# Performance work log

Hardware: AMD Instinct MI355X
Metric: run time of the kernel (lower is better)

The kernel has to match this reference:

```python
import jax, jax.numpy as jnp
import numpy as np

H = 1024        # hidden_size
E = 8           # num_experts
K = 2           # experts_per_token
I = 1024        # intermediate_size (mlp1 outputs 2*I, interleaved gate/linear)
N = 4096        # n_tokens
ALPHA = 1.702
LIMIT = 7.0
EPS = 1e-5


def setup_inputs() -> dict:
    key = jax.random.key(0)
    ks = jax.random.split(key, 5)
    x = jax.random.normal(ks[0], (N, H), jnp.float32)
    norm_scale = jnp.ones((H,), jnp.float32)
    gate_w = jax.random.normal(ks[1], (H, E), jnp.float32) * 0.02
    gate_b = jnp.zeros((E,), jnp.float32)
    mlp1_w = jax.random.normal(ks[2], (E, 2 * I, H), jnp.float32) * 0.02
    mlp1_b = jnp.zeros((E, 2 * I), jnp.float32)
    mlp2_w = jax.random.normal(ks[3], (E, H, I), jnp.float32) * 0.02
    mlp2_b = jnp.zeros((E, H), jnp.float32)
    return {"x": x, "norm_scale": norm_scale, "gate_w": gate_w, "gate_b": gate_b,
            "mlp1_w": mlp1_w, "mlp1_b": mlp1_b, "mlp2_w": mlp2_w, "mlp2_b": mlp2_b}


def _swiglu(h):
    # even indices = gate, odd indices = linear (interleaved)
    x_g = jnp.minimum(h[..., ::2], LIMIT)           # clip gate above only
    x_l = jnp.clip(h[..., 1::2], -LIMIT, LIMIT)     # clip linear both sides
    return x_g * jax.nn.sigmoid(ALPHA * x_g) * (x_l + 1.0)


def reference(x, norm_scale, gate_w, gate_b, mlp1_w, mlp1_b, mlp2_w, mlp2_b):
    # RMSNorm (fp32)
    t = x * jax.lax.rsqrt(jnp.mean(x * x, axis=-1, keepdims=True) + EPS) * norm_scale
    # Router: top-k gating with softmax over selected logits
    g = t @ gate_w + gate_b                          # [N, E]
    logits, idx = jax.lax.top_k(g, K)                # [N, K]
    w = jax.nn.softmax(logits, axis=-1)              # [N, K]
    n = x.shape[0]
    # Scatter routing weights into dense combine matrix [N, E]
    # (top_k indices are unique per row, so .set is exact)
    combine = jnp.zeros((n, E), x.dtype).at[jnp.arange(n)[:, None], idx].set(w)
    # Per-expert SwiGLU MLP over all tokens, weighted combine + residual.
    # Loop over the small fixed expert count (E=8); avoids materializing the
    # huge [N, K, 2I, H] gathered-weight tensor from the original gather path.
    out = x
    for e in range(E):
        h1 = _swiglu(t @ mlp1_w[e].T + mlp1_b[e])    # [N, I]
        h2 = h1 @ mlp2_w[e].T + mlp2_b[e]            # [N, H]
        out = out + combine[:, e:e + 1] * h2
    return out
```

## Files before the change

kernel.cpp:

```cpp
#include <hip/hip_runtime.h>
#include <hip/hip_bf16.h>
#include <stdint.h>

#define HDIM 1024
#define NEXP 8
#define TOPK 2
#define IDIM 1024
#define TWO_I 2048
#define ALPHA 1.702f
#define LIMIT 7.0f
#define EPS 1e-5f

#define BM 128
#define BN 128
#define BK 64

typedef __attribute__((ext_vector_type(8))) short bf16x8;
typedef __attribute__((ext_vector_type(4))) float f32x4;

typedef __attribute__((address_space(1))) const uint32_t g_u32;
typedef __attribute__((address_space(3))) uint32_t l_u32;

__device__ __forceinline__ void load_lds16(const void* g, void* l) {
    __builtin_amdgcn_global_load_lds((g_u32*)g, (l_u32*)l, 16, 0, 0);
}

__device__ __forceinline__ ushort f2bf(float f) {
    union { float f; uint32_t u; } v{f};
    uint32_t u = v.u;
    return (ushort)((u + 0x7fffu + ((u >> 16) & 1u)) >> 16);
}

__global__ __launch_bounds__(256) void k_f32_to_bf16(const float* __restrict__ src,
                                                     ushort* __restrict__ dst, int n4) {
    int i = blockIdx.x * blockDim.x + threadIdx.x;
    int stride = gridDim.x * blockDim.x;
    for (; i < n4; i += stride) {
        float4 v = reinterpret_cast<const float4*>(src)[i];
        ushort4 o;
        o.x = f2bf(v.x); o.y = f2bf(v.y); o.z = f2bf(v.z); o.w = f2bf(v.w);
        reinterpret_cast<ushort4*>(dst)[i] = o;
    }
}

__global__ __launch_bounds__(256) void k_conv_w1(const float* __restrict__ src,
                                                 ushort* __restrict__ dst) {
    const int b = blockIdx.x;
    const int e = b >> 11;
    const int j = b & 2047;
    const int dj = ((j & 1) << 10) | (j >> 1);
    const float4* s = reinterpret_cast<const float4*>(src + (size_t)b * HDIM);
    ushort4* d = reinterpret_cast<ushort4*>(dst + ((size_t)e * TWO_I + dj) * HDIM);
    float4 v = s[threadIdx.x];
    ushort4 o;
    o.x = f2bf(v.x); o.y = f2bf(v.y); o.z = f2bf(v.z); o.w = f2bf(v.w);
    d[threadIdx.x] = o;
}

__global__ __launch_bounds__(256) void k_norm_router(
    const float* __restrict__ x, const float* __restrict__ scale,
    const float* __restrict__ gw, const float* __restrict__ gb,
    ushort* __restrict__ t_bf, float* __restrict__ route_w,
    int* __restrict__ counts, int* __restrict__ bucket, int n_tok)
{
    const int n = blockIdx.x;
    const int tid = threadIdx.x;
    const int lane = tid & 63, wid = tid >> 6;

    __shared__ float red[4];
    __shared__ float gred[4][NEXP];

    const float4 xv = reinterpret_cast<const float4*>(x + (size_t)n * HDIM)[tid];
    float ss = xv.x * xv.x + xv.y * xv.y + xv.z * xv.z + xv.w * xv.w;
    #pragma unroll
    for (int off = 32; off; off >>= 1) ss += __shfl_down(ss, off, 64);
    if (lane == 0) red[wid] = ss;
    __syncthreads();
    const float tot = red[0] + red[1] + red[2] + red[3];
    const float rms = rsqrtf(tot / (float)HDIM + EPS);

    const float4 sv = reinterpret_cast<const float4*>(scale)[tid];
    float t0 = xv.x * rms * sv.x;
    float t1 = xv.y * rms * sv.y;
    float t2 = xv.z * rms * sv.z;
    float t3 = xv.w * rms * sv.w;

    ushort4 tb;
    tb.x = f2bf(t0); tb.y = f2bf(t1); tb.z = f2bf(t2); tb.w = f2bf(t3);
    reinterpret_cast<ushort4*>(t_bf + (size_t)n * HDIM)[tid] = tb;

    float g[NEXP];
    #pragma unroll
    for (int e = 0; e < NEXP; ++e) g[e] = 0.f;
    const float tv[4] = {t0, t1, t2, t3};
    const float4* gwv = reinterpret_cast<const float4*>(gw);
    #pragma unroll
    for (int j = 0; j < 4; ++j) {
        const int h = tid * 4 + j;
        const float4 a = gwv[h * 2 + 0];
        const float4 b = gwv[h * 2 + 1];
        g[0] += tv[j] * a.x; g[1] += tv[j] * a.y; g[2] += tv[j] * a.z; g[3] += tv[j] * a.w;
        g[4] += tv[j] * b.x; g[5] += tv[j] * b.y; g[6] += tv[j] * b.z; g[7] += tv[j] * b.w;
    }
    #pragma unroll
    for (int e = 0; e < NEXP; ++e) {
        #pragma unroll
        for (int off = 32; off; off >>= 1) g[e] += __shfl_down(g[e], off, 64);
    }
    if (lane == 0) {
        #pragma unroll
        for (int e = 0; e < NEXP; ++e) gred[wid][e] = g[e];
    }
    __syncthreads();

    if (tid == 0) {
        float gg[NEXP];
        #pragma unroll
        for (int e = 0; e < NEXP; ++e)
            gg[e] = gred[0][e] + gred[1][e] + gred[2][e] + gred[3][e] + gb[e];
        int i0 = 0; float l0 = gg[0];
        #pragma unroll
        for (int e = 1; e < NEXP; ++e) if (gg[e] > l0) { l0 = gg[e]; i0 = e; }
        int i1 = -1; float l1 = -3.4e38f;
        #pragma unroll
        for (int e = 0; e < NEXP; ++e) if (e != i0 && gg[e] > l1) { l1 = gg[e]; i1 = e; }
        const float w0 = 1.f / (1.f + __expf(l1 - l0));
        const float w1 = 1.f - w0;
        route_w[n * 2 + 0] = w0;
        route_w[n * 2 + 1] = w1;
        int p0 = atomicAdd(&counts[i0], 1);
        bucket[i0 * n_tok + p0] = n * 2 + 0;
        int p1 = atomicAdd(&counts[i1], 1);
        bucket[i1 * n_tok + p1] = n * 2 + 1;
    }
}

__global__ __launch_bounds__(256) void k_gemm1(
    const ushort* __restrict__ tA, const ushort* __restrict__ w1bf,
    const float* __restrict__ b1,
    const int* __restrict__ counts, const int* __restrict__ bucket,
    ushort* __restrict__ h1, int n_tok, int rt_max)
{
    const int bx = blockIdx.x;
    const int rt = bx >> 7;
    const int e  = (bx >> 4) & 7;
    const int jt = bx & 15;
    const int cnt = counts[e];
    if (rt * BM >= cnt) return;

    __shared__ __align__(16) ushort As[2][BM * BK];
    __shared__ __align__(16) ushort Bs[2][BN * BK];

    const int tid = threadIdx.x;
    const int lane = tid & 63, wid = tid >> 6;
    const int wm = wid >> 1, wn = wid & 1;

    int tokrow[4];
    #pragma unroll
    for (int it = 0; it < 4; ++it) {
        int pos = rt * BM + it * 32 + (tid >> 3);
        tokrow[it] = bucket[e * n_tok + min(pos, cnt - 1)] >> 1;
    }
    const ushort* wbase = w1bf + (size_t)e * TWO_I * HDIM;
    const ushort* bsrc[4];
    #pragma unroll
    for (int it = 0; it < 4; ++it) {
        int br = it * 32 + (tid >> 3);
        int G = br >> 4, r16 = br & 15;
        int half = (G >> 1) & 1;
        int sub = ((G >> 2) << 1) | (G & 1);
        int srcrow = half * IDIM + jt * 64 + sub * 16 + r16;
        bsrc[it] = wbase + (size_t)srcrow * HDIM;
    }
    const int swz = (((tid & 7) ^ ((tid >> 3) & 7)) * 8);

    f32x4 acc[4][4];
    #pragma unroll
    for (int mi = 0; mi < 4; ++mi)
        #pragma unroll
        for (int ni = 0; ni < 4; ++ni) acc[mi][ni] = (f32x4)0.f;

    auto stage = [&](int buf, int kt) {
        const int k0 = kt * BK + swz;
        #pragma unroll
        for (int it = 0; it < 4; ++it)
            load_lds16(tA + (size_t)tokrow[it] * HDIM + k0, &As[buf][(it * 32 + wid * 8) * BK]);
        #pragma unroll
        for (int it = 0; it < 4; ++it)
            load_lds16(bsrc[it] + k0, &Bs[buf][(it * 32 + wid * 8) * BK]);
    };
    auto compute = [&](int buf) {
        #pragma unroll
        for (int kk = 0; kk < 2; ++kk) {
            bf16x8 a[4], b[4];
            #pragma unroll
            for (int mi = 0; mi < 4; ++mi) {
                int r = wm * 64 + mi * 16 + (lane & 15);
                int off = r * BK + (((kk * 4 + (lane >> 4)) ^ (lane & 7)) * 8);
                a[mi] = *reinterpret_cast<const bf16x8*>(&As[buf][off]);
            }
            #pragma unroll
            for (int ni = 0; ni < 4; ++ni) {
                int r = wn * 64 + ni * 16 + (lane & 15);
                int off = r * BK + (((kk * 4 + (lane >> 4)) ^ (lane & 7)) * 8);
                b[ni] = *reinterpret_cast<const bf16x8*>(&Bs[buf][off]);
            }
            #pragma unroll
            for (int mi = 0; mi < 4; ++mi)
                #pragma unroll
                for (int ni = 0; ni < 4; ++ni)
                    acc[mi][ni] = __builtin_amdgcn_mfma_f32_16x16x32_bf16(a[mi], b[ni], acc[mi][ni], 0, 0, 0);
        }
    };

    stage(0, 0);
    __syncthreads();
    int cur = 0;
    for (int kt = 0; kt < HDIM / BK; ++kt) {
        if (kt + 1 < HDIM / BK) stage(cur ^ 1, kt + 1);
        compute(cur);
        __syncthreads();
        cur ^= 1;
    }

    int ent[4][4];
    #pragma unroll
    for (int mi = 0; mi < 4; ++mi)
        #pragma unroll
        for (int r = 0; r < 4; ++r) {
            int pos = rt * BM + wm * 64 + mi * 16 + (lane >> 4) * 4 + r;
            ent[mi][r] = (pos < cnt) ? bucket[e * n_tok + pos] : -1;
        }
    #pragma unroll
    for (int ni = 0; ni < 2; ++ni) {
        const int col = jt * 64 + (wn * 2 + ni) * 16 + (lane & 15);
        const float bg = b1[e * TWO_I + 2 * col];
        const float bl = b1[e * TWO_I + 2 * col + 1];
        #pragma unroll
        for (int mi = 0; mi < 4; ++mi) {
            const f32x4 vg = acc[mi][ni];
            const f32x4 vl = acc[mi][ni + 2];
            #pragma unroll
            for (int r = 0; r < 4; ++r) {
                if (ent[mi][r] >= 0) {
                    const float xg = fminf(vg[r] + bg, LIMIT);
                    const float xl = fminf(fmaxf(vl[r] + bl, -LIMIT), LIMIT);
                    const float s = 1.f / (1.f + __expf(-ALPHA * xg));
                    h1[(size_t)ent[mi][r] * IDIM + col] = f2bf(xg * s * (xl + 1.f));
                }
            }
        }
    }
}

__global__ __launch_bounds__(256) void k_gemm2(
    const ushort* __restrict__ h1, const ushort* __restrict__ w2bf,
    const float* __restrict__ b2, const float* __restrict__ route_w,
    const int* __restrict__ counts, const int* __restrict__ bucket,
    float* __restrict__ contrib, int n_tok, int rt_max)
{
    const int bx = blockIdx.x;
    const int rt = bx >> 6;
    const int e  = (bx >> 3) & 7;
    const int ct = bx & 7;
    const int cnt = counts[e];
    if (rt * BM >= cnt) return;
    const int c0 = ct * BN;

    __shared__ __align__(16) ushort As[2][BM * BK];
    __shared__ __align__(16) ushort Bs[2][BN * BK];

    const int tid = threadIdx.x;
    const int lane = tid & 63, wid = tid >> 6;
    const int wm = wid >> 1, wn = wid & 1;

    int rowent[4];
    #pragma unroll
    for (int it = 0; it < 4; ++it) {
        int pos = rt * BM + it * 32 + (tid >> 3);
        rowent[it] = bucket[e * n_tok + min(pos, cnt - 1)];
    }
    const ushort* wB = w2bf + (size_t)e * HDIM * IDIM;
    const int swz = (((tid & 7) ^ ((tid >> 3) & 7)) * 8);

    f32x4 acc[4][4];
    #pragma unroll
    for (int mi = 0; mi < 4; ++mi)
        #pragma unroll
        for (int ni = 0; ni < 4; ++ni) acc[mi][ni] = (f32x4)0.f;

    auto stage = [&](int buf, int kt) {
        const int k0 = kt * BK + swz;
        #pragma unroll
        for (int it = 0; it < 4; ++it)
            load_lds16(h1 + (size_t)rowent[it] * IDIM + k0, &As[buf][(it * 32 + wid * 8) * BK]);
        #pragma unroll
        for (int it = 0; it < 4; ++it)
            load_lds16(wB + (size_t)(c0 + it * 32 + (tid >> 3)) * IDIM + k0, &Bs[buf][(it * 32 + wid * 8) * BK]);
    };
    auto compute = [&](int buf) {
        #pragma unroll
        for (int kk = 0; kk < 2; ++kk) {
            bf16x8 a[4], b[4];
            #pragma unroll
            for (int mi = 0; mi < 4; ++mi) {
                int r = wm * 64 + mi * 16 + (lane & 15);
                int off = r * BK + (((kk * 4 + (lane >> 4)) ^ (lane & 7)) * 8);
                a[mi] = *reinterpret_cast<const bf16x8*>(&As[buf][off]);
            }
            #pragma unroll
            for (int ni = 0; ni < 4; ++ni) {
                int r = wn * 64 + ni * 16 + (lane & 15);
                int off = r * BK + (((kk * 4 + (lane >> 4)) ^ (lane & 7)) * 8);
                b[ni] = *reinterpret_cast<const bf16x8*>(&Bs[buf][off]);
            }
            #pragma unroll
            for (int mi = 0; mi < 4; ++mi)
                #pragma unroll
                for (int ni = 0; ni < 4; ++ni)
                    acc[mi][ni] = __builtin_amdgcn_mfma_f32_16x16x32_bf16(a[mi], b[ni], acc[mi][ni], 0, 0, 0);
        }
    };

    stage(0, 0);
    __syncthreads();
    int cur = 0;
    for (int kt = 0; kt < IDIM / BK; ++kt) {
        if (kt + 1 < IDIM / BK) stage(cur ^ 1, kt + 1);
        compute(cur);
        __syncthreads();
        cur ^= 1;
    }

    int ent[4][4];
    float wgt[4][4];
    #pragma unroll
    for (int mi = 0; mi < 4; ++mi)
        #pragma unroll
        for (int r = 0; r < 4; ++r) {
            int pos = rt * BM + wm * 64 + mi * 16 + (lane >> 4) * 4 + r;
            if (pos < cnt) {
                ent[mi][r] = bucket[e * n_tok + pos];
                wgt[mi][r] = route_w[ent[mi][r]];
            } else ent[mi][r] = -1;
        }
    #pragma unroll
    for (int ni = 0; ni < 4; ++ni) {
        const int c = c0 + wn * 64 + ni * 16 + (lane & 15);
        const float bc = b2[e * HDIM + c];
        #pragma unroll
        for (int mi = 0; mi < 4; ++mi) {
            const f32x4 v = acc[mi][ni];
            #pragma unroll
            for (int r = 0; r < 4; ++r) {
                if (ent[mi][r] >= 0) {
                    const int tok = ent[mi][r] >> 1, slot = ent[mi][r] & 1;
                    contrib[((size_t)slot * n_tok + tok) * HDIM + c] = wgt[mi][r] * (v[r] + bc);
                }
            }
        }
    }
}

__global__ __launch_bounds__(256) void k_combine(
    const float* __restrict__ x, const float* __restrict__ contrib,
    float* __restrict__ out, int n4, int slot_stride4)
{
    int i = blockIdx.x * blockDim.x + threadIdx.x;
    if (i >= n4) return;
    float4 xv = reinterpret_cast<const float4*>(x)[i];
    float4 c0 = reinterpret_cast<const float4*>(contrib)[i];
    float4 c1 = reinterpret_cast<const float4*>(contrib)[i + slot_stride4];
    float4 o;
    o.x = xv.x + c0.x + c1.x;
    o.y = xv.y + c0.y + c1.y;
    o.z = xv.z + c0.z + c1.z;
    o.w = xv.w + c0.w + c1.w;
    reinterpret_cast<float4*>(out)[i] = o;
}

extern "C" void kernel_launch(void* const* d_in, const int* in_sizes, int n_in,
                              void* d_out, int out_size, void* d_ws, size_t ws_size,
                              hipStream_t stream) {
    const float* x    = (const float*)d_in[0];
    const float* nsc  = (const float*)d_in[1];
    const float* gw   = (const float*)d_in[2];
    const float* gb   = (const float*)d_in[3];
    const float* w1   = (const float*)d_in[4];
    const float* b1   = (const float*)d_in[5];
    const float* w2   = (const float*)d_in[6];
    const float* b2   = (const float*)d_in[7];
    float* out = (float*)d_out;

    const int N = in_sizes[0] / HDIM;
    const int rt_max = (N + BM - 1) / BM;

    uintptr_t p = (uintptr_t)d_ws;
    auto carve = [&p](size_t bytes) { uintptr_t q = p; p += (bytes + 255) & ~(size_t)255; return q; };
    ushort* t_bf    = (ushort*)carve((size_t)N * HDIM * 2);
    ushort* w1bf    = (ushort*)carve((size_t)NEXP * TWO_I * HDIM * 2);
    ushort* w2bf    = (ushort*)carve((size_t)NEXP * HDIM * IDIM * 2);
    ushort* h1      = (ushort*)carve((size_t)N * TOPK * IDIM * 2);
    float*  contrib = (float*)carve((size_t)TOPK * N * HDIM * 4);
    float*  route_w = (float*)carve((size_t)N * TOPK * 4);
    int*    bucket  = (int*)carve((size_t)NEXP * N * 4);
    int*    counts  = (int*)carve(256);

    hipMemsetAsync(counts, 0, NEXP * sizeof(int), stream);

    k_conv_w1<<<NEXP * TWO_I, 256, 0, stream>>>(w1, w1bf);
    const int n4w2 = NEXP * HDIM * IDIM / 4;
    k_f32_to_bf16<<<2048, 256, 0, stream>>>(w2, w2bf, n4w2);

    k_norm_router<<<N, 256, 0, stream>>>(x, nsc, gw, gb, t_bf, route_w, counts, bucket, N);

    k_gemm1<<<rt_max * NEXP * (TWO_I / BN), 256, 0, stream>>>(t_bf, w1bf, b1, counts, bucket, h1, N, rt_max);
    k_gemm2<<<rt_max * NEXP * (HDIM / BN), 256, 0, stream>>>(h1, w2bf, b2, route_w, counts, bucket, contrib, N, rt_max);

    const int n4 = N * HDIM / 4;
    k_combine<<<(n4 + 255) / 256, 256, 0, stream>>>(x, contrib, out, n4, n4);
}
```

Measured before the change: 407.7 us.

## Split norm/router into wave-per-token gating and ballot-based bucketing kernel

The fused norm+router kernel, which used one 256-thread block per token and two global atomics per token, is replaced by two kernels. The first processes one token per wave, uses xor-shuffle reductions with no shared memory or block syncs, and writes expert indices to a new buffer. The second builds the per-expert buckets with wave ballots, a prefix scan in shared memory, and one atomic per expert per block. This removes heavy global atomic contention on eight counters and the per-token block syncs, at the cost of an extra kernel launch and a small intermediate buffer. The bucket order is now deterministic per block.

Measured after the change: 337.7 us. 1.21x faster.

```diff
diff --git a/kernel.cpp b/kernel.cpp
--- a/kernel.cpp
+++ b/kernel.cpp
@@ -57,81 +57,138 @@
     d[threadIdx.x] = o;
 }
 
-__global__ __launch_bounds__(256) void k_norm_router(
+__global__ __launch_bounds__(256) void k_norm_gate(
     const float* __restrict__ x, const float* __restrict__ scale,
     const float* __restrict__ gw, const float* __restrict__ gb,
     ushort* __restrict__ t_bf, float* __restrict__ route_w,
-    int* __restrict__ counts, int* __restrict__ bucket, int n_tok)
+    int* __restrict__ eidx, int n_tok)
 {
-    const int n = blockIdx.x;
+    const int tok = blockIdx.x * 4 + (threadIdx.x >> 6);
+    if (tok >= n_tok) return;
+    const int lane = threadIdx.x & 63;
+
+    const float4* xr = reinterpret_cast<const float4*>(x + (size_t)tok * HDIM);
+    const float4* sr = reinterpret_cast<const float4*>(scale);
+    float4 xv[4], sv[4];
+    #pragma unroll
+    for (int j = 0; j < 4; ++j) { xv[j] = xr[lane + 64 * j]; sv[j] = sr[lane + 64 * j]; }
+
+    float ss = 0.f;
+    #pragma unroll
+    for (int j = 0; j < 4; ++j)
+        ss += xv[j].x * xv[j].x + xv[j].y * xv[j].y + xv[j].z * xv[j].z + xv[j].w * xv[j].w;
+    #pragma unroll
+    for (int off = 1; off < 64; off <<= 1) ss += __shfl_xor(ss, off, 64);
+    const float rms = rsqrtf(ss / (float)HDIM + EPS);
+
+    float t[4][4];
+    ushort4* tw = reinterpret_cast<ushort4*>(t_bf + (size_t)tok * HDIM);
+    #pragma unroll
+    for (int j = 0; j < 4; ++j) {
+        t[j][0] = xv[j].x * rms * sv[j].x;
+        t[j][1] = xv[j].y * rms * sv[j].y;
+        t[j][2] = xv[j].z * rms * sv[j].z;
+        t[j][3] = xv[j].w * rms * sv[j].w;
+        ushort4 o;
+        o.x = f2bf(t[j][0]); o.y = f2bf(t[j][1]); o.z = f2bf(t[j][2]); o.w = f2bf(t[j][3]);
+        tw[lane + 64 * j] = o;
+    }
+
+    float g[NEXP];
+    #pragma unroll
+    for (int e = 0; e < NEXP; ++e) g[e] = 0.f;
+    const float4* gwv = reinterpret_cast<const float4*>(gw);
+    #pragma unroll
+    for (int j = 0; j < 4; ++j) {
+        #pragma unroll
+        for (int c = 0; c < 4; ++c) {
+            const int h = (lane + 64 * j) * 4 + c;
+            const float tv = t[j][c];
+            const float4 a = gwv[h * 2 + 0];
+            const float4 b = gwv[h * 2 + 1];
+            g[0] += tv * a.x; g[1] += tv * a.y; g[2] += tv * a.z; g[3] += tv * a.w;
+            g[4] += tv * b.x; g[5] += tv * b.y; g[6] += tv * b.z; g[7] += tv * b.w;
+        }
+    }
+    #pragma unroll
+    for (int e = 0; e < NEXP; ++e) {
+        #pragma unroll
+        for (int off = 1; off < 64; off <<= 1) g[e] += __shfl_xor(g[e], off, 64);
+    }
+
+    if (lane == 0) {
+        float gg[NEXP];
+        #pragma unroll
+        for (int e = 0; e < NEXP; ++e) gg[e] = g[e] + gb[e];
+        int i0 = 0; float l0 = gg[0];
+        #pragma unroll
+        for (int e = 1; e < NEXP; ++e) if (gg[e] > l0) { l0 = gg[e]; i0 = e; }
+        int i1 = -1; float l1 = -3.4e38f;
+        #pragma unroll
+        for (int e = 0; e < NEXP; ++e) if (e != i0 && gg[e] > l1) { l1 = gg[e]; i1 = e; }
+        const float w0 = 1.f / (1.f + __expf(l1 - l0));
+        route_w[tok * 2 + 0] = w0;
+        route_w[tok * 2 + 1] = 1.f - w0;
+        eidx[tok * 2 + 0] = i0;
+        eidx[tok * 2 + 1] = i1;
+    }
+}
+
+#define BKT_BLOCKS 8
+__global__ __launch_bounds__(256) void k_bucket(
+    const int* __restrict__ eidx, int* __restrict__ counts,
+    int* __restrict__ bucket, int n_tok)
+{
+    const int total = 2 * n_tok;
+    const int per_block = total / BKT_BLOCKS;
+    const int rounds = per_block / 256;
+    const int base_ent = blockIdx.x * per_block;
     const int tid = threadIdx.x;
     const int lane = tid & 63, wid = tid >> 6;
 
-    __shared__ float red[4];
-    __shared__ float gred[4][NEXP];
-
-    const float4 xv = reinterpret_cast<const float4*>(x + (size_t)n * HDIM)[tid];
-    float ss = xv.x * xv.x + xv.y * xv.y + xv.z * xv.z + xv.w * xv.w;
-    #pragma unroll
-    for (int off = 32; off; off >>= 1) ss += __shfl_down(ss, off, 64);
-    if (lane == 0) red[wid] = ss;
+    __shared__ int wavecnt[4][4][NEXP];
+    __shared__ int cum[4][4][NEXP];
+    __shared__ int gbase[NEXP];
+
+    int me[4], rank[4];
+    #pragma unroll
+    for (int r = 0; r < 4; ++r) {
+        const int ent = base_ent + r * 256 + tid;
+        const int e = (r < rounds) ? eidx[ent] : -1;
+        me[r] = e;
+        #pragma unroll
+        for (int ex = 0; ex < NEXP; ++ex) {
+            unsigned long long m = __ballot(e == ex);
+            if (e == ex) rank[r] = __popcll(m & ((1ull << lane) - 1ull));
+            if (lane == 0) wavecnt[r][wid][ex] = (int)__popcll(m);
+        }
+    }
     __syncthreads();
-    const float tot = red[0] + red[1] + red[2] + red[3];
-    const float rms = rsqrtf(tot / (float)HDIM + EPS);
-
-    const float4 sv = reinterpret_cast<const float4*>(scale)[tid];
-    float t0 = xv.x * rms * sv.x;
-    float t1 = xv.y * rms * sv.y;
-    float t2 = xv.z * rms * sv.z;
-    float t3 = xv.w * rms * sv.w;
-
-    ushort4 tb;
-    tb.x = f2bf(t0); tb.y = f2bf(t1); tb.z = f2bf(t2); tb.w = f2bf(t3);
-    reinterpret_cast<ushort4*>(t_bf + (size_t)n * HDIM)[tid] = tb;
-
-    float g[NEXP];
-    #pragma unroll
-    for (int e = 0; e < NEXP; ++e) g[e] = 0.f;
-    const float tv[4] = {t0, t1, t2, t3};
-    const float4* gwv = reinterpret_cast<const float4*>(gw);
-    #pragma unroll
-    for (int j = 0; j < 4; ++j) {
-        const int h = tid * 4 + j;
-        const float4 a = gwv[h * 2 + 0];
-        const float4 b = gwv[h * 2 + 1];
-        g[0] += tv[j] * a.x; g[1] += tv[j] * a.y; g[2] += tv[j] * a.z; g[3] += tv[j] * a.w;
-        g[4] += tv[j] * b.x; g[5] += tv[j] * b.y; g[6] += tv[j] * b.z; g[7] += tv[j] * b.w;
-    }
-    #pragma unroll
-    for (int e = 0; e < NEXP; ++e) {
-        #pragma unroll
-        for (int off = 32; off; off >>= 1) g[e] += __shfl_down(g[e], off, 64);
-    }
-    if (lane == 0) {
-        #pragma unroll
-        for (int e = 0; e < NEXP; ++e) gred[wid][e] = g[e];
+
+    if (tid < 4 * 4 * NEXP) {
+        const int e = tid & 7, w = (tid >> 3) & 3, r = tid >> 5;
+        int s = 0;
+        for (int rr = 0; rr < 4; ++rr)
+            for (int ww = 0; ww < 4; ++ww)
+                if (rr < r || (rr == r && ww < w)) s += wavecnt[rr][ww][e];
+        cum[r][w][e] = s;
     }
     __syncthreads();
-
-    if (tid == 0) {
-        float gg[NEXP];
-        #pragma unroll
-        for (int e = 0; e < NEXP; ++e)
-            gg[e] = gred[0][e] + gred[1][e] + gred[2][e] + gred[3][e] + gb[e];
-        int i0 = 0; float l0 = gg[0];
-        #pragma unroll
-        for (int e = 1; e < NEXP; ++e) if (gg[e] > l0) { l0 = gg[e]; i0 = e; }
-        int i1 = -1; float l1 = -3.4e38f;
-        #pragma unroll
-        for (int e = 0; e < NEXP; ++e) if (e != i0 && gg[e] > l1) { l1 = gg[e]; i1 = e; }
-        const float w0 = 1.f / (1.f + __expf(l1 - l0));
-        const float w1 = 1.f - w0;
-        route_w[n * 2 + 0] = w0;
-        route_w[n * 2 + 1] = w1;
-        int p0 = atomicAdd(&counts[i0], 1);
-        bucket[i0 * n_tok + p0] = n * 2 + 0;
-        int p1 = atomicAdd(&counts[i1], 1);
-        bucket[i1 * n_tok + p1] = n * 2 + 1;
+    if (tid < NEXP) {
+        int tot = 0;
+        for (int rr = 0; rr < 4; ++rr)
+            for (int ww = 0; ww < 4; ++ww) tot += wavecnt[rr][ww][tid];
+        gbase[tid] = atomicAdd(&counts[tid], tot);
+    }
+    __syncthreads();
+
+    #pragma unroll
+    for (int r = 0; r < 4; ++r) {
+        const int e = me[r];
+        if (e >= 0) {
+            const int ent = base_ent + r * 256 + tid;
+            bucket[e * n_tok + gbase[e] + cum[r][wid][e] + rank[r]] = ent;
+        }
     }
 }
 
@@ -404,6 +461,7 @@
     float*  contrib = (float*)carve((size_t)TOPK * N * HDIM * 4);
     float*  route_w = (float*)carve((size_t)N * TOPK * 4);
     int*    bucket  = (int*)carve((size_t)NEXP * N * 4);
+    int*    eidx    = (int*)carve((size_t)N * TOPK * 4);
     int*    counts  = (int*)carve(256);
 
     hipMemsetAsync(counts, 0, NEXP * sizeof(int), stream);
@@ -412,7 +470,8 @@
     const int n4w2 = NEXP * HDIM * IDIM / 4;
     k_f32_to_bf16<<<2048, 256, 0, stream>>>(w2, w2bf, n4w2);
 
-    k_norm_router<<<N, 256, 0, stream>>>(x, nsc, gw, gb, t_bf, route_w, counts, bucket, N);
+    k_norm_gate<<<(N + 3) / 4, 256, 0, stream>>>(x, nsc, gw, gb, t_bf, route_w, eidx, N);
+    k_bucket<<<BKT_BLOCKS, 256, 0, stream>>>(eidx, counts, bucket, N);
 
     k_gemm1<<<rt_max * NEXP * (TWO_I / BN), 256, 0, stream>>>(t_bf, w1bf, b1, counts, bucket, h1, N, rt_max);
     k_gemm2<<<rt_max * NEXP * (HDIM / BN), 256, 0, stream>>>(h1, w2bf, b2, route_w, counts, bucket, contrib, N, rt_max);
```
